# Optimization experiments

Hardware: AMD Instinct MI355X
Metric: run time of the kernel (lower is better)

The kernel has to match this reference:

```python
import jax, jax.numpy as jnp
import numpy as np

N = 32768        # atoms
INV = 256        # irreps_in[inv_field].dim (scalar latent width)
MUL = 32         # input eq multiplicity: '32x1o'
VOUT = 4         # output eq multiplicity: '4x1o'
HID = 512        # ScalarMLPFunction latent dims [512, 512]
INV_OUT = 2      # inv_out_irreps '2x0e'
TYPES = 32       # num_types
EPS = 1e-10


def _mlp(x, w1, w2, w3):
    # ScalarMLPFunction: Linear(+1/sqrt(fan_in) norm) -> SiLU -> ... -> Linear
    h = jax.nn.silu((x @ w1) * (1.0 / np.sqrt(w1.shape[0])))
    h = jax.nn.silu((h @ w2) * (1.0 / np.sqrt(w2.shape[0])))
    return (h @ w3) * (1.0 / np.sqrt(w3.shape[0]))


def setup_inputs() -> dict:
    key = jax.random.key(0)
    ks = jax.random.split(key, 10)
    inv_features = jax.random.normal(ks[0], (N, INV), dtype=jnp.float32)
    eq_features = jax.random.normal(ks[1], (N, MUL, 3), dtype=jnp.float32)
    atom_types = jax.random.randint(ks[2], (N, 1), 0, TYPES, dtype=jnp.int32)
    # hypernetwork (final_latent): INV -> 512 -> 512 -> MUL*VOUT
    w1_lat = jax.random.normal(ks[3], (INV, HID), dtype=jnp.float32)
    w2_lat = jax.random.normal(ks[4], (HID, HID), dtype=jnp.float32)
    w3_lat = jax.random.normal(ks[5], (HID, MUL * VOUT), dtype=jnp.float32)
    # final_readout: INV -> 512 -> 512 -> INV_OUT
    w1_ro = jax.random.normal(ks[6], (INV, HID), dtype=jnp.float32)
    w2_ro = jax.random.normal(ks[7], (HID, HID), dtype=jnp.float32)
    w3_ro = jax.random.normal(ks[8], (HID, INV_OUT), dtype=jnp.float32)
    # atom_type2bond_lengths parameter, init to ones as in the module
    bond_lengths = jnp.ones((TYPES, VOUT, 1), dtype=jnp.float32)
    return dict(inv_features=inv_features, eq_features=eq_features,
                atom_types=atom_types, w1_lat=w1_lat, w2_lat=w2_lat,
                w3_lat=w3_lat, w1_ro=w1_ro, w2_ro=w2_ro, w3_ro=w3_ro,
                bond_lengths=bond_lengths)


def reference(inv_features, eq_features, atom_types, w1_lat, w2_lat, w3_lat,
              w1_ro, w2_ro, w3_ro, bond_lengths):
    # hypernet-generated per-atom weights for the equivariant Linear
    weights = _mlp(inv_features, w1_lat, w2_lat, w3_lat)          # [N, MUL*VOUT]
    weights = weights.reshape(-1, MUL, VOUT)                      # [N, u, v]
    inv_out = _mlp(inv_features, w1_ro, w2_ro, w3_ro)             # [N, INV_OUT]
    # e3nn Linear '32x1o -> 4x1o', shared_weights=False, path norm 1/sqrt(mul_in)
    eq = jnp.einsum('num,nuv->nvm', eq_features, weights) * (1.0 / np.sqrt(MUL))
    # norm -> divide -> nan_to_num
    norm = jnp.linalg.norm(eq, axis=-1, keepdims=True)            # [N, VOUT, 1]
    eq = jnp.nan_to_num(eq / (norm + EPS), nan=0.0)
    # per-atom-type bond-length scale (gather-multiply)
    eq = eq * bond_lengths[atom_types[:, 0]]                      # [N, VOUT, 3]
    return inv_out, eq
```

## Files before the change

### kernel.cpp

```cpp
#include <hip/hip_runtime.h>
#include <hip/hip_bf16.h>

#define N_ATOMS 32768

typedef __attribute__((ext_vector_type(4))) float f32x4;
typedef __attribute__((ext_vector_type(8))) short bf16x8;
typedef unsigned short u16;

__device__ __forceinline__ u16 f2b(float f) {
    union { __hip_bfloat16 b; u16 u; } c;
    c.b = __float2bfloat16(f);
    return c.u;
}
__device__ __forceinline__ float b2f(u16 u) {
    union { unsigned int i; float f; } c;
    c.i = ((unsigned int)u) << 16;
    return c.f;
}

#define GLDS16(src, dst) __builtin_amdgcn_global_load_lds( \
    (const __attribute__((address_space(1))) void*)(src),  \
    (__attribute__((address_space(3))) void*)(dst), 16, 0, 0)

__global__ void __launch_bounds__(256) setup_kernel(
        const float* __restrict__ x, u16* __restrict__ xhi, u16* __restrict__ xlo,
        const float* __restrict__ w1l, const float* __restrict__ w2l,
        const float* __restrict__ w3l, const float* __restrict__ w1r,
        const float* __restrict__ w2r,
        u16* __restrict__ W1LThi, u16* __restrict__ W1LTlo, u16* __restrict__ W1RT,
        u16* __restrict__ W2LThi, u16* __restrict__ W2LTlo, u16* __restrict__ W2RT,
        u16* __restrict__ W3LThi, u16* __restrict__ W3LTlo,
        float* __restrict__ out_inv) {
    int bid = blockIdx.x;
    if (bid < 4096) {
        size_t i = (size_t)(bid * 256 + threadIdx.x) * 8;
        float4 v0 = *(const float4*)(x + i);
        float4 v1 = *(const float4*)(x + i + 4);
        float v[8] = {v0.x, v0.y, v0.z, v0.w, v1.x, v1.y, v1.z, v1.w};
        bf16x8 rh, rl;
#pragma unroll
        for (int j = 0; j < 8; ++j) {
            u16 h = f2b(v[j]);
            rh[j] = (short)h;
            rl[j] = (short)f2b(v[j] - b2f(h));
        }
        *(bf16x8*)(xhi + i) = rh;
        *(bf16x8*)(xlo + i) = rl;
    } else if (bid < 7424) {
        int i = (bid - 4096) * 256 + threadIdx.x;
        if (i < 131072) {
            int n = i >> 8, k = i & 255;
            float v = w1l[k * 512 + n];
            u16 h = f2b(v);
            W1LThi[i] = h;
            W1LTlo[i] = f2b(v - b2f(h));
        } else if (i < 262144) {
            int j = i - 131072;
            int n = j >> 8, k = j & 255;
            W1RT[j] = f2b(w1r[k * 512 + n]);
        } else if (i < 524288) {
            int j = i - 262144;
            int n = j >> 9, k = j & 511;
            float v = w2l[k * 512 + n];
            u16 h = f2b(v);
            W2LThi[j] = h;
            W2LTlo[j] = f2b(v - b2f(h));
        } else if (i < 786432) {
            int j = i - 524288;
            int n = j >> 9, k = j & 511;
            W2RT[j] = f2b(w2r[k * 512 + n]);
        } else if (i < 851968) {
            int j = i - 786432;
            int n = j >> 9, k = j & 511;
            float v = w3l[k * 128 + n];
            u16 h = f2b(v);
            W3LThi[j] = h;
            W3LTlo[j] = f2b(v - b2f(h));
        }
    } else {
        int i = (bid - 7424) * 256 + threadIdx.x;
        *(float4*)(out_inv + i * 4) = float4{0.f, 0.f, 0.f, 0.f};
    }
}

template<int NSEG, int NF, bool SILU, int OUTK>
__device__ __forceinline__ void gemm_body(
        u16* __restrict__ smem,
        const u16* __restrict__ Ahi, const u16* __restrict__ Alo,
        const u16* __restrict__ Bhi, const u16* __restrict__ Blo,
        void* __restrict__ Chi, void* __restrict__ Clo,
        int ldc, int K, float scale,
        const float* __restrict__ e_w3, float* __restrict__ e_out,
        int bid, int nwg, int GX) {
    constexpr int LBSZ = NF * 64 * 64;
    u16* const lA0 = smem;
    u16* const lB0 = smem + 32768;
    const int tid = threadIdx.x;
    const int lane = tid & 63;
    const int wid = tid >> 6;
    const int wm = wid >> 2;
    const int wn = wid & 3;
    const int rlane = lane & 15;
    const int kc = lane >> 4;
    const int cps = rlane & 7;
    const int srow = tid >> 3;
    const int scp = tid & 7;

    const int wg = (bid & 7) * (nwg >> 3) + (bid >> 3);
    const int bn = (wg % GX) * (NF * 64);
    const int bm = (wg / GX) * 256;

    const int kt = K >> 6;
    const int NT = NSEG * kt;

    auto stageA = [&](int t, int buf) {
        int seg = (NSEG == 1) ? 0 : ((t >= kt) + (t >= 2 * kt));
        const u16* As = (NSEG == 1) ? Ahi : (seg == 1 ? Alo : Ahi);
        int k0 = (t - seg * kt) << 6;
        u16* la = lA0 + buf * 16384;
#pragma unroll
        for (int call = 0; call < 4; ++call) {
            int row = call * 64 + srow;
            int c = scp ^ (row & 7);
            GLDS16(As + (size_t)(bm + row) * K + k0 + c * 8, la + (size_t)(row * 64 + scp * 8));
        }
    };
    auto stageB = [&](int t, int buf) {
        int seg = (NSEG == 1) ? 0 : ((t >= kt) + (t >= 2 * kt));
        const u16* Bs = (NSEG == 1) ? Bhi : (seg == 2 ? Blo : Bhi);
        int k0 = (t - seg * kt) << 6;
        u16* lb = lB0 + buf * LBSZ;
#pragma unroll
        for (int call = 0; call < NF; ++call) {
            int row = call * 64 + srow;
            int c = scp ^ (row & 7);
            GLDS16(Bs + (size_t)(bn + row) * K + k0 + c * 8, lb + (size_t)(row * 64 + scp * 8));
        }
    };

    f32x4 acc[8][NF] = {};

    stageA(0, 0);
    stageB(0, 0);
    asm volatile("s_waitcnt vmcnt(0)" ::: "memory");
    __builtin_amdgcn_s_barrier();

    for (int t = 0; t < NT; ++t) {
        const int cur = t & 1, nxt = cur ^ 1;
        const bool pf = (t + 1 < NT);
        const u16* la = lA0 + cur * 16384;
        const u16* lb = lB0 + cur * LBSZ;
#pragma unroll
        for (int ks = 0; ks < 2; ++ks) {
            bf16x8 af[8], bfr[NF];
            const int cp = (ks * 4 + kc) ^ cps;
#pragma unroll
            for (int m = 0; m < 8; ++m) {
                int row = wm * 128 + m * 16 + rlane;
                af[m] = *(const bf16x8*)&la[row * 64 + cp * 8];
            }
#pragma unroll
            for (int n = 0; n < NF; ++n) {
                int row = wn * (NF * 16) + n * 16 + rlane;
                bfr[n] = *(const bf16x8*)&lb[row * 64 + cp * 8];
            }
            if (pf) {
                if (ks == 0) stageA(t + 1, nxt);
                else         stageB(t + 1, nxt);
            }
            asm volatile("s_waitcnt lgkmcnt(0)" ::: "memory");
            __builtin_amdgcn_sched_barrier(0);
            __builtin_amdgcn_s_setprio(1);
#pragma unroll
            for (int m = 0; m < 8; ++m)
#pragma unroll
                for (int n = 0; n < NF; ++n)
                    acc[m][n] = __builtin_amdgcn_mfma_f32_16x16x32_bf16(af[m], bfr[n], acc[m][n], 0, 0, 0);
            __builtin_amdgcn_s_setprio(0);
        }
        asm volatile("s_waitcnt vmcnt(0)" ::: "memory");
        __builtin_amdgcn_s_barrier();
    }

    const int g = lane >> 4;

    if constexpr (OUTK == 3) {
        const float s512f = 0.04419417382415922f;
        float wj0[NF], wj1[NF];
#pragma unroll
        for (int n = 0; n < NF; ++n) {
            int gc = bn + wn * (NF * 16) + n * 16 + rlane;
            wj0[n] = e_w3[gc * 2] * s512f;
            wj1[n] = e_w3[gc * 2 + 1] * s512f;
        }
#pragma unroll
        for (int m = 0; m < 8; ++m)
#pragma unroll
            for (int r = 0; r < 4; ++r) {
                float s0 = 0.f, s1 = 0.f;
#pragma unroll
                for (int n = 0; n < NF; ++n) {
                    float v = acc[m][n][r] * scale;
                    v = v / (1.0f + __expf(-v));
                    s0 = fmaf(v, wj0[n], s0);
                    s1 = fmaf(v, wj1[n], s1);
                }
#pragma unroll
                for (int off = 1; off < 16; off <<= 1) {
                    s0 += __shfl_xor(s0, off);
                    s1 += __shfl_xor(s1, off);
                }
                if (rlane == 0) {
                    int row = bm + wm * 128 + m * 16 + g * 4 + r;
                    atomicAdd(&e_out[row * 2], s0);
                    atomicAdd(&e_out[row * 2 + 1], s1);
                }
            }
    } else {
#pragma unroll
        for (int m = 0; m < 8; ++m) {
            int grow0 = bm + wm * 128 + m * 16 + (g << 2);
#pragma unroll
            for (int n = 0; n < NF; ++n) {
                int gcol = bn + wn * (NF * 16) + n * 16 + rlane;
#pragma unroll
                for (int r = 0; r < 4; ++r) {
                    float v = acc[m][n][r] * scale;
                    if constexpr (SILU) v = v / (1.0f + __expf(-v));
                    size_t idx = (size_t)(grow0 + r) * ldc + gcol;
                    if constexpr (OUTK == 0) {
                        ((float*)Chi)[idx] = v;
                    } else if constexpr (OUTK == 1) {
                        ((u16*)Chi)[idx] = f2b(v);
                    } else {
                        u16 h = f2b(v);
                        ((u16*)Chi)[idx] = h;
                        ((u16*)Clo)[idx] = f2b(v - b2f(h));
                    }
                }
            }
        }
    }
}

static constexpr float S256 = 0.0625f;
static constexpr float S512 = 0.04419417382415922f;

__global__ void __launch_bounds__(512, 2) gemm_l1(
        const u16* __restrict__ XHI, const u16* __restrict__ XLO,
        const u16* __restrict__ W1LThi, const u16* __restrict__ W1LTlo,
        const u16* __restrict__ W1RT,
        u16* __restrict__ H1Lhi, u16* __restrict__ H1Llo, u16* __restrict__ H1R) {
    __shared__ __align__(16) u16 smem[65536];
    int bid = blockIdx.x;
    if (bid < 256)
        gemm_body<3, 4, true, 2>(smem, XHI, XLO, W1LThi, W1LTlo, H1Lhi, H1Llo,
                                 512, 256, S256, nullptr, nullptr, bid, 256, 2);
    else
        gemm_body<1, 4, true, 1>(smem, XHI, nullptr, W1RT, nullptr, H1R, nullptr,
                                 512, 256, S256, nullptr, nullptr, bid - 256, 256, 2);
}

__global__ void __launch_bounds__(512, 2) gemm_l2(
        const u16* __restrict__ H1Lhi, const u16* __restrict__ H1Llo,
        const u16* __restrict__ W2LThi, const u16* __restrict__ W2LTlo,
        const u16* __restrict__ H1R, const u16* __restrict__ W2RT,
        u16* __restrict__ H2Lhi, u16* __restrict__ H2Llo,
        const float* __restrict__ w3r, float* __restrict__ out_inv) {
    __shared__ __align__(16) u16 smem[65536];
    int bid = blockIdx.x;
    if (bid < 256)
        gemm_body<3, 4, true, 2>(smem, H1Lhi, H1Llo, W2LThi, W2LTlo, H2Lhi, H2Llo,
                                 512, 512, S512, nullptr, nullptr, bid, 256, 2);
    else
        gemm_body<1, 4, true, 3>(smem, H1R, nullptr, W2RT, nullptr, nullptr, nullptr,
                                 0, 512, S512, w3r, out_inv, bid - 256, 256, 2);
}

__global__ void __launch_bounds__(512, 2) gemm_l3(
        const u16* __restrict__ H2Lhi, const u16* __restrict__ H2Llo,
        const u16* __restrict__ W3LThi, const u16* __restrict__ W3LTlo,
        float* __restrict__ WGT) {
    __shared__ __align__(16) u16 smem[40960];
    gemm_body<3, 1, false, 0>(smem, H2Lhi, H2Llo, W3LThi, W3LTlo, WGT, nullptr,
                              128, 512, S512, nullptr, nullptr, (int)blockIdx.x, 256, 2);
}

__global__ void eq_kernel(const float* __restrict__ eqf, const float* __restrict__ wgt,
                          const int* __restrict__ types, const float* __restrict__ bond,
                          float* __restrict__ out) {
    int t = blockIdx.x * 256 + threadIdx.x;
    int n = t >> 2, v = t & 3;
    const float* e = eqf + (size_t)n * 96;
    const float* w = wgt + (size_t)n * 128 + v;
    float a0 = 0.f, a1 = 0.f, a2 = 0.f;
#pragma unroll
    for (int u = 0; u < 32; ++u) {
        float wv = w[u * 4];
        a0 = fmaf(e[u * 3 + 0], wv, a0);
        a1 = fmaf(e[u * 3 + 1], wv, a1);
        a2 = fmaf(e[u * 3 + 2], wv, a2);
    }
    const float s = 0.17677669529663687f;
    a0 *= s; a1 *= s; a2 *= s;
    float norm = sqrtf(a0 * a0 + a1 * a1 + a2 * a2) + 1e-10f;
    float bl = bond[types[n] * 4 + v];
    float r0 = a0 / norm, r1 = a1 / norm, r2 = a2 / norm;
    if (isnan(r0)) r0 = 0.f;
    if (isnan(r1)) r1 = 0.f;
    if (isnan(r2)) r2 = 0.f;
    out[(size_t)n * 12 + v * 3 + 0] = r0 * bl;
    out[(size_t)n * 12 + v * 3 + 1] = r1 * bl;
    out[(size_t)n * 12 + v * 3 + 2] = r2 * bl;
}

extern "C" void kernel_launch(void* const* d_in, const int* in_sizes, int n_in,
                              void* d_out, int out_size, void* d_ws, size_t ws_size,
                              hipStream_t stream) {
    const float* inv  = (const float*)d_in[0];
    const float* eqf  = (const float*)d_in[1];
    const int*   typs = (const int*)d_in[2];
    const float* w1l  = (const float*)d_in[3];
    const float* w2l  = (const float*)d_in[4];
    const float* w3l  = (const float*)d_in[5];
    const float* w1r  = (const float*)d_in[6];
    const float* w2r  = (const float*)d_in[7];
    const float* w3r  = (const float*)d_in[8];
    const float* bond = (const float*)d_in[9];

    char* ws = (char*)d_ws;
    const size_t MB = 1024 * 1024, KB = 1024;
    u16* XHI   = (u16*)(ws);
    u16* XLO   = (u16*)(ws + 16 * MB);
    u16* H1R   = (u16*)(ws + 32 * MB);
    u16* H1Lhi = (u16*)(ws + 64 * MB);
    u16* H1Llo = (u16*)(ws + 96 * MB);
    u16* H2Lhi = (u16*)(ws);
    u16* H2Llo = (u16*)(ws + 128 * MB);
    float* WGT = (float*)(ws + 32 * MB);
    char* wb = ws + 160 * MB;
    u16* W1LThi = (u16*)(wb);
    u16* W1LTlo = (u16*)(wb + 256 * KB);
    u16* W1RT   = (u16*)(wb + 512 * KB);
    u16* W2LThi = (u16*)(wb + 768 * KB);
    u16* W2LTlo = (u16*)(wb + 1280 * KB);
    u16* W2RT   = (u16*)(wb + 1792 * KB);
    u16* W3LThi = (u16*)(wb + 2304 * KB);
    u16* W3LTlo = (u16*)(wb + 2432 * KB);

    float* out_inv = (float*)d_out;
    float* out_eq  = (float*)d_out + N_ATOMS * 2;

    setup_kernel<<<dim3(7488), dim3(256), 0, stream>>>(
        inv, XHI, XLO, w1l, w2l, w3l, w1r, w2r,
        W1LThi, W1LTlo, W1RT, W2LThi, W2LTlo, W2RT, W3LThi, W3LTlo, out_inv);
    gemm_l1<<<dim3(512), dim3(512), 0, stream>>>(
        XHI, XLO, W1LThi, W1LTlo, W1RT, H1Lhi, H1Llo, H1R);
    gemm_l2<<<dim3(512), dim3(512), 0, stream>>>(
        H1Lhi, H1Llo, W2LThi, W2LTlo, H1R, W2RT, H2Lhi, H2Llo, w3r, out_inv);
    gemm_l3<<<dim3(256), dim3(512), 0, stream>>>(H2Lhi, H2Llo, W3LThi, W3LTlo, WGT);
    eq_kernel<<<dim3(512), dim3(256), 0, stream>>>(eqf, WGT, typs, bond, out_eq);
}
```

Before: 190.6 us.

## Split layer-2 into separate kernels and split-precision layer-3 into three partial GEMMs

Layer 2 now runs as two kernels, readout first and then the latent path, instead of one mixed launch that branched on block index. Layer 3's three-pass split-bf16 GEMM (hi*hi, lo*hi, hi*lo) becomes 384 blocks, one single-pass GEMM per precision segment, each writing its own fp32 partial buffer. The eq kernel then sums the three partial weight tensors. The aim is more parallelism in the small layer-3 GEMM, at the cost of an extra launch and triple the weight-tensor writes and reads.

```diff
diff --git a/kernel.cpp b/kernel.cpp
--- a/kernel.cpp
+++ b/kernel.cpp
@@ -261,29 +261,35 @@
                                  512, 256, S256, nullptr, nullptr, bid - 256, 256, 2);
 }
 
-__global__ void __launch_bounds__(512, 2) gemm_l2(
+__global__ void __launch_bounds__(512, 2) gemm_l2lat(
         const u16* __restrict__ H1Lhi, const u16* __restrict__ H1Llo,
         const u16* __restrict__ W2LThi, const u16* __restrict__ W2LTlo,
+        u16* __restrict__ H2Lhi, u16* __restrict__ H2Llo) {
+    __shared__ __align__(16) u16 smem[65536];
+    gemm_body<3, 4, true, 2>(smem, H1Lhi, H1Llo, W2LThi, W2LTlo, H2Lhi, H2Llo,
+                             512, 512, S512, nullptr, nullptr, (int)blockIdx.x, 256, 2);
+}
+
+__global__ void __launch_bounds__(512, 2) gemm_l2ro(
         const u16* __restrict__ H1R, const u16* __restrict__ W2RT,
-        u16* __restrict__ H2Lhi, u16* __restrict__ H2Llo,
         const float* __restrict__ w3r, float* __restrict__ out_inv) {
     __shared__ __align__(16) u16 smem[65536];
-    int bid = blockIdx.x;
-    if (bid < 256)
-        gemm_body<3, 4, true, 2>(smem, H1Lhi, H1Llo, W2LThi, W2LTlo, H2Lhi, H2Llo,
-                                 512, 512, S512, nullptr, nullptr, bid, 256, 2);
-    else
-        gemm_body<1, 4, true, 3>(smem, H1R, nullptr, W2RT, nullptr, nullptr, nullptr,
-                                 0, 512, S512, w3r, out_inv, bid - 256, 256, 2);
-}
-
-__global__ void __launch_bounds__(512, 2) gemm_l3(
+    gemm_body<1, 4, true, 3>(smem, H1R, nullptr, W2RT, nullptr, nullptr, nullptr,
+                             0, 512, S512, w3r, out_inv, (int)blockIdx.x, 256, 2);
+}
+
+__global__ void __launch_bounds__(512, 1) gemm_l3s(
         const u16* __restrict__ H2Lhi, const u16* __restrict__ H2Llo,
         const u16* __restrict__ W3LThi, const u16* __restrict__ W3LTlo,
-        float* __restrict__ WGT) {
-    __shared__ __align__(16) u16 smem[40960];
-    gemm_body<3, 1, false, 0>(smem, H2Lhi, H2Llo, W3LThi, W3LTlo, WGT, nullptr,
-                              128, 512, S512, nullptr, nullptr, (int)blockIdx.x, 256, 2);
+        float* __restrict__ WGTp) {
+    __shared__ __align__(16) u16 smem[49152];
+    int seg = blockIdx.x >> 7;
+    int b = blockIdx.x & 127;
+    const u16* A = (seg == 1) ? H2Llo : H2Lhi;
+    const u16* B = (seg == 2) ? W3LTlo : W3LThi;
+    float* C = WGTp + (size_t)seg * (N_ATOMS * 128);
+    gemm_body<1, 2, false, 0>(smem, A, nullptr, B, nullptr, C, nullptr,
+                              128, 512, S512, nullptr, nullptr, b, 128, 1);
 }
 
 __global__ void eq_kernel(const float* __restrict__ eqf, const float* __restrict__ wgt,
@@ -292,11 +298,13 @@
     int t = blockIdx.x * 256 + threadIdx.x;
     int n = t >> 2, v = t & 3;
     const float* e = eqf + (size_t)n * 96;
-    const float* w = wgt + (size_t)n * 128 + v;
+    const float* w0 = wgt + (size_t)n * 128 + v;
+    const float* w1 = w0 + (size_t)N_ATOMS * 128;
+    const float* w2 = w1 + (size_t)N_ATOMS * 128;
     float a0 = 0.f, a1 = 0.f, a2 = 0.f;
 #pragma unroll
     for (int u = 0; u < 32; ++u) {
-        float wv = w[u * 4];
+        float wv = w0[u * 4] + w1[u * 4] + w2[u * 4];
         a0 = fmaf(e[u * 3 + 0], wv, a0);
         a1 = fmaf(e[u * 3 + 1], wv, a1);
         a2 = fmaf(e[u * 3 + 2], wv, a2);
@@ -337,7 +345,7 @@
     u16* H1Llo = (u16*)(ws + 96 * MB);
     u16* H2Lhi = (u16*)(ws);
     u16* H2Llo = (u16*)(ws + 128 * MB);
-    float* WGT = (float*)(ws + 32 * MB);
+    float* WGTp = (float*)(ws + 32 * MB);
     char* wb = ws + 160 * MB;
     u16* W1LThi = (u16*)(wb);
     u16* W1LTlo = (u16*)(wb + 256 * KB);
@@ -356,8 +364,10 @@
         W1LThi, W1LTlo, W1RT, W2LThi, W2LTlo, W2RT, W3LThi, W3LTlo, out_inv);
     gemm_l1<<<dim3(512), dim3(512), 0, stream>>>(
         XHI, XLO, W1LThi, W1LTlo, W1RT, H1Lhi, H1Llo, H1R);
-    gemm_l2<<<dim3(512), dim3(512), 0, stream>>>(
-        H1Lhi, H1Llo, W2LThi, W2LTlo, H1R, W2RT, H2Lhi, H2Llo, w3r, out_inv);
-    gemm_l3<<<dim3(256), dim3(512), 0, stream>>>(H2Lhi, H2Llo, W3LThi, W3LTlo, WGT);
-    eq_kernel<<<dim3(512), dim3(256), 0, stream>>>(eqf, WGT, typs, bond, out_eq);
-}
+    gemm_l2ro<<<dim3(256), dim3(512), 0, stream>>>(H1R, W2RT, w3r, out_inv);
+    gemm_l2lat<<<dim3(256), dim3(512), 0, stream>>>(
+        H1Lhi, H1Llo, W2LThi, W2LTlo, H2Lhi, H2Llo);
+    gemm_l3s<<<dim3(384), dim3(512), 0, stream>>>(
+        H2Lhi, H2Llo, W3LThi, W3LTlo, WGTp);
+    eq_kernel<<<dim3(512), dim3(256), 0, stream>>>(eqf, WGTp, typs, bond, out_eq);
+}
```

Measured after the change: 195.9 us. +2.8%, slower.
